# Optimization experiments

Hardware: AMD Instinct MI355X
Metric: run time of the kernel (lower is better)

## Reference

```python
import jax, jax.numpy as jnp
import numpy as np


def setup_inputs() -> dict:
    key = jax.random.key(0)
    ks = jax.random.split(key, 18)
    V, E, H, T = 32000, 512, 1024, 256
    s_e = 1.0 / np.sqrt(E)
    s_h = 1.0 / np.sqrt(H)
    inp = {
        "encoding": jax.random.normal(ks[0], (1, H), jnp.float32),
        "tokens": jax.random.randint(ks[1], (T,), 0, V),
        "embedding": jax.random.normal(ks[2], (V, E), jnp.float32),
        "wzx_w": jax.random.normal(ks[3], (H, E), jnp.float32) * s_e,
        "wzx_b": jax.random.normal(ks[4], (H,), jnp.float32) * s_e,
        "wrx_w": jax.random.normal(ks[5], (H, E), jnp.float32) * s_e,
        "wrx_b": jax.random.normal(ks[6], (H,), jnp.float32) * s_e,
        "whx_w": jax.random.normal(ks[7], (H, E), jnp.float32) * s_e,
        "whx_b": jax.random.normal(ks[8], (H,), jnp.float32) * s_e,
        "wzh_w": jax.random.normal(ks[9], (H, H), jnp.float32) * s_h,
        "wzh_b": jax.random.normal(ks[10], (H,), jnp.float32) * s_h,
        "wrh_w": jax.random.normal(ks[11], (H, H), jnp.float32) * s_h,
        "wrh_b": jax.random.normal(ks[12], (H,), jnp.float32) * s_h,
        "whh_w": jax.random.normal(ks[13], (H, H), jnp.float32) * s_h,
        "whh_b": jax.random.normal(ks[14], (H,), jnp.float32) * s_h,
        "out_w": jax.random.normal(ks[15], (V, H), jnp.float32) * s_h,
        "out_b": jax.random.normal(ks[16], (V,), jnp.float32) * s_h,
    }
    return inp


def reference(encoding, tokens, embedding,
              wzx_w, wzx_b, wrx_w, wrx_b, whx_w, whx_b,
              wzh_w, wzh_b, wrh_w, wrh_b, whh_w, whh_b,
              out_w, out_b):
    # Teacher-forced GRU decode: tokens[t] is the 'previous word' fed at step t.
    def step(h, tok):
        e = embedding[tok][None, :]                                   # [1, E]
        z = jax.nn.sigmoid(e @ wzx_w.T + wzx_b + h @ wzh_w.T + wzh_b)  # [1, H]
        r = jax.nn.sigmoid(e @ wrx_w.T + wrx_b + h @ wrh_w.T + wrh_b)
        h_prime = jnp.tanh(e @ whx_w.T + whx_b + (r * h) @ whh_w.T + whh_b)
        h_new = (1.0 - z) * h + z * h_prime
        logits = h_new @ out_w.T + out_b                               # [1, V]
        return h_new, logits

    _, output_vectors = jax.lax.scan(step, encoding, tokens)          # [T, 1, V]
    pred_ids = jnp.argmax(output_vectors, axis=-1)                    # [T, 1]
    return output_vectors, pred_ids
```

## Files before the change

kernel.cpp:

```cpp
#include <hip/hip_runtime.h>
#include <hip/hip_bf16.h>
#include <math.h>

constexpr int T_STEPS = 256;
constexpr int HDIM    = 1024;
constexpr int EDIM    = 512;
constexpr int VDIM    = 32000;

#define RG     128
#define RROWS  8

constexpr size_t WS_BZ     = 0;
constexpr size_t WS_BR     = WS_BZ + (size_t)T_STEPS * HDIM;
constexpr size_t WS_A      = WS_BR + (size_t)T_STEPS * HDIM;
constexpr size_t WS_HPACK  = WS_A  + (size_t)T_STEPS * HDIM;
constexpr size_t WS_RHPACK = WS_HPACK + (size_t)2 * (T_STEPS + 1) * HDIM;
constexpr size_t WS_HSEQ   = WS_BZ;
constexpr size_t WS_HSEQB  = WS_BR;

typedef __attribute__((ext_vector_type(8))) short short8;
typedef __attribute__((ext_vector_type(4))) float f32x4;

__device__ __forceinline__ float sigmoidf_(float x) { return 1.0f / (1.0f + __expf(-x)); }

__device__ __forceinline__ unsigned long long pack_tv(int tag, float v) {
  return ((unsigned long long)(unsigned)tag << 32) | (unsigned long long)__float_as_uint(v);
}

__device__ __forceinline__ unsigned short f2bf(float f) {
  unsigned u = __float_as_uint(f);
  return (unsigned short)((u + 0x7FFFu + ((u >> 16) & 1u)) >> 16);
}

__global__ __launch_bounds__(256) void k_init(const float* __restrict__ enc, float* __restrict__ ws) {
  unsigned long long* hpack  = (unsigned long long*)(ws + WS_HPACK);
  unsigned long long* rhpack = (unsigned long long*)(ws + WS_RHPACK);
  const int b = blockIdx.x, tid = threadIdx.x;
  if (b == 0) {
    for (int i = tid; i < HDIM; i += 256) hpack[i] = pack_tv(1, enc[i]);
  } else if (b <= T_STEPS) {
    unsigned long long* row = hpack + (size_t)b * HDIM;
    for (int i = tid; i < HDIM; i += 256) row[i] = 0ULL;
  } else {
    for (int i = tid; i < HDIM; i += 256) rhpack[i] = 0ULL;
  }
}

__global__ __launch_bounds__(256) void k_xproj(
    const int* __restrict__ tokens, const float* __restrict__ emb,
    const float* __restrict__ wzx, const float* __restrict__ wrx, const float* __restrict__ whx,
    const float* __restrict__ bzx, const float* __restrict__ bzh,
    const float* __restrict__ brx, const float* __restrict__ brh,
    const float* __restrict__ bhx, const float* __restrict__ bhh,
    float* __restrict__ ws) {
  __shared__ __align__(16) float es[16][EDIM];
  const int b   = blockIdx.x;
  const int t0  = (b & 15) * 16;
  const int c   = b >> 4;
  const int tid = threadIdx.x;

  {
    int row = tid >> 4;
    int kc  = (tid & 15) * 32;
    int tok = tokens[t0 + row];
    const float4* ep = (const float4*)(emb + (size_t)tok * EDIM + kc);
    float4* dst = (float4*)&es[row][kc];
    #pragma unroll
    for (int q = 0; q < 8; q++) dst[q] = ep[q];
  }
  __syncthreads();

  const int mat = c >> 2;
  const int j   = (c & 3) * 256 + tid;
  const float* W; const float* b1; const float* b2; float* Xout;
  if (mat == 0)      { W = wzx; b1 = bzx; b2 = bzh; Xout = ws + WS_BZ; }
  else if (mat == 1) { W = wrx; b1 = brx; b2 = brh; Xout = ws + WS_BR; }
  else               { W = whx; b1 = bhx; b2 = bhh; Xout = ws + WS_A;  }

  const float4* wp = (const float4*)(W + (size_t)j * EDIM);
  const float bias = b1[j] + b2[j];
  float acc[16];
  #pragma unroll
  for (int tt = 0; tt < 16; tt++) acc[tt] = 0.0f;

  for (int k4 = 0; k4 < EDIM / 4; k4++) {
    float4 w = wp[k4];
    #pragma unroll
    for (int tt = 0; tt < 16; tt++) {
      float4 e4 = *(const float4*)&es[tt][k4 * 4];
      acc[tt] += w.x * e4.x + w.y * e4.y + w.z * e4.z + w.w * e4.w;
    }
  }
  #pragma unroll
  for (int tt = 0; tt < 16; tt++)
    Xout[(size_t)(t0 + tt) * HDIM + j] = acc[tt] + bias;
}

__global__ __launch_bounds__(256) void k_recur(
    const float* __restrict__ wzh, const float* __restrict__ wrh, const float* __restrict__ whh,
    float* __restrict__ ws) {
  const int g    = blockIdx.x;
  const int tid  = threadIdx.x;
  const int lane = tid & 63;
  const int wv   = tid >> 6;
  const float* Bz = ws + WS_BZ;
  const float* Br = ws + WS_BR;
  const float* Aa = ws + WS_A;
  float* hseq = ws + WS_HSEQ;
  unsigned short* hseqb = (unsigned short*)(ws + WS_HSEQB);
  unsigned long long* hpack  = (unsigned long long*)(ws + WS_HPACK);
  unsigned long long* rhpack = (unsigned long long*)(ws + WS_RHPACK);

  const int j0 = 4 * tid;
  const int r0 = g * RROWS;

  float4 wz[RROWS], wr[RROWS], wh[RROWS];
  #pragma unroll
  for (int k = 0; k < RROWS; k++) {
    wz[k] = *(const float4*)(wzh + (size_t)(r0 + k) * HDIM + j0);
    wr[k] = *(const float4*)(wrh + (size_t)(r0 + k) * HDIM + j0);
    wh[k] = *(const float4*)(whh + (size_t)(r0 + k) * HDIM + j0);
  }

  __shared__ float redA[4][2 * RROWS];
  __shared__ float redB[4][RROWS];
  __shared__ float zs[RROWS];
  __shared__ float hloc[RROWS];
  if (tid < RROWS)
    hloc[tid] = __uint_as_float((unsigned)hpack[r0 + tid]);
  __syncthreads();

  for (int t = 0; t < T_STEPS; t++) {
    float bz_pre = 0.0f, br_pre = 0.0f, a_pre = 0.0f;
    if (tid < RROWS) {
      bz_pre = Bz[(size_t)t * HDIM + r0 + tid];
      a_pre  = Aa[(size_t)t * HDIM + r0 + tid];
    } else if (tid < 2 * RROWS) {
      br_pre = Br[(size_t)t * HDIM + r0 + (tid - RROWS)];
    }
    const unsigned long long ex = (unsigned long long)(unsigned)(t + 1);

    float hv0, hv1, hv2, hv3;
    {
      const unsigned long long* hp = hpack + (size_t)t * HDIM + j0;
      unsigned long long w0, w1, w2, w3;
      int it = 0;
      for (;;) {
        w0 = __hip_atomic_load(hp + 0, __ATOMIC_RELAXED, __HIP_MEMORY_SCOPE_AGENT);
        if ((w0 >> 32) == ex) break;
        if (++it > (1 << 20)) break;
        __builtin_amdgcn_s_sleep(2);
      }
      for (;;) {
        w1 = __hip_atomic_load(hp + 1, __ATOMIC_RELAXED, __HIP_MEMORY_SCOPE_AGENT);
        w2 = __hip_atomic_load(hp + 2, __ATOMIC_RELAXED, __HIP_MEMORY_SCOPE_AGENT);
        w3 = __hip_atomic_load(hp + 3, __ATOMIC_RELAXED, __HIP_MEMORY_SCOPE_AGENT);
        if (((w1 >> 32) == ex) & ((w2 >> 32) == ex) & ((w3 >> 32) == ex)) break;
        if (++it > (1 << 20)) break;
        __builtin_amdgcn_s_sleep(1);
      }
      hv0 = __uint_as_float((unsigned)w0);
      hv1 = __uint_as_float((unsigned)w1);
      hv2 = __uint_as_float((unsigned)w2);
      hv3 = __uint_as_float((unsigned)w3);
    }

    float pz[RROWS], pr[RROWS];
    #pragma unroll
    for (int k = 0; k < RROWS; k++) {
      pz[k] = wz[k].x * hv0 + wz[k].y * hv1 + wz[k].z * hv2 + wz[k].w * hv3;
      pr[k] = wr[k].x * hv0 + wr[k].y * hv1 + wr[k].z * hv2 + wr[k].w * hv3;
    }
    #pragma unroll
    for (int m = 32; m >= 1; m >>= 1) {
      #pragma unroll
      for (int k = 0; k < RROWS; k++) {
        pz[k] += __shfl_xor(pz[k], m);
        pr[k] += __shfl_xor(pr[k], m);
      }
    }
    if (lane == 0) {
      #pragma unroll
      for (int k = 0; k < RROWS; k++) { redA[wv][k] = pz[k]; redA[wv][RROWS + k] = pr[k]; }
    }
    __syncthreads();
    if (tid < RROWS) {
      float u = redA[0][tid] + redA[1][tid] + redA[2][tid] + redA[3][tid];
      zs[tid] = sigmoidf_(bz_pre + u);
    } else if (tid < 2 * RROWS) {
      int k = tid - RROWS;
      float u = redA[0][tid] + redA[1][tid] + redA[2][tid] + redA[3][tid];
      float r = sigmoidf_(br_pre + u);
      float rh = r * hloc[k];
      __hip_atomic_store(&rhpack[r0 + k], pack_tv(t + 1, rh),
                         __ATOMIC_RELAXED, __HIP_MEMORY_SCOPE_AGENT);
    }

    float rv0, rv1, rv2, rv3;
    {
      const unsigned long long* rp = rhpack + j0;
      unsigned long long w0, w1, w2, w3;
      int it = 0;
      for (;;) {
        w0 = __hip_atomic_load(rp + 0, __ATOMIC_RELAXED, __HIP_MEMORY_SCOPE_AGENT);
        if ((w0 >> 32) == ex) break;
        if (++it > (1 << 20)) break;
        __builtin_amdgcn_s_sleep(2);
      }
      for (;;) {
        w1 = __hip_atomic_load(rp + 1, __ATOMIC_RELAXED, __HIP_MEMORY_SCOPE_AGENT);
        w2 = __hip_atomic_load(rp + 2, __ATOMIC_RELAXED, __HIP_MEMORY_SCOPE_AGENT);
        w3 = __hip_atomic_load(rp + 3, __ATOMIC_RELAXED, __HIP_MEMORY_SCOPE_AGENT);
        if (((w1 >> 32) == ex) & ((w2 >> 32) == ex) & ((w3 >> 32) == ex)) break;
        if (++it > (1 << 20)) break;
        __builtin_amdgcn_s_sleep(1);
      }
      rv0 = __uint_as_float((unsigned)w0);
      rv1 = __uint_as_float((unsigned)w1);
      rv2 = __uint_as_float((unsigned)w2);
      rv3 = __uint_as_float((unsigned)w3);
    }

    float ph[RROWS];
    #pragma unroll
    for (int k = 0; k < RROWS; k++)
      ph[k] = wh[k].x * rv0 + wh[k].y * rv1 + wh[k].z * rv2 + wh[k].w * rv3;
    #pragma unroll
    for (int m = 32; m >= 1; m >>= 1) {
      #pragma unroll
      for (int k = 0; k < RROWS; k++) ph[k] += __shfl_xor(ph[k], m);
    }
    if (lane == 0) {
      #pragma unroll
      for (int k = 0; k < RROWS; k++) redB[wv][k] = ph[k];
    }
    __syncthreads();
    if (tid < RROWS) {
      float v  = redB[0][tid] + redB[1][tid] + redB[2][tid] + redB[3][tid];
      float z  = zs[tid];
      float hk = hloc[tid];
      float hp_ = tanhf(a_pre + v);
      float hn = (1.0f - z) * hk + z * hp_;
      hloc[tid] = hn;
      __hip_atomic_store(&hpack[(size_t)(t + 1) * HDIM + r0 + tid], pack_tv(t + 2, hn),
                         __ATOMIC_RELAXED, __HIP_MEMORY_SCOPE_AGENT);
      hseq[(size_t)t * HDIM + r0 + tid] = hn;
      hseqb[(size_t)t * HDIM + r0 + tid] = f2bf(hn);
    }
  }
}

__global__ __launch_bounds__(256) void k_gemm(
    const unsigned short* __restrict__ Abf, const float* __restrict__ outw,
    const float* __restrict__ outb, float* __restrict__ out) {
  const int tid  = threadIdx.x;
  const int lane = tid & 63;
  const int wv   = tid >> 6;
  const int n0   = blockIdx.x * 128;
  const int rA   = lane & 15;
  const int kg   = lane >> 4;

  f32x4 acc[4][8];
  #pragma unroll
  for (int i = 0; i < 4; i++)
    #pragma unroll
    for (int j = 0; j < 8; j++) acc[i][j] = (f32x4){0.f, 0.f, 0.f, 0.f};

  const int mbase = wv * 64 + rA;

  for (int k0 = 0; k0 < HDIM; k0 += 32) {
    const int ks = k0 + kg * 8;
    short8 afr[4];
    #pragma unroll
    for (int i = 0; i < 4; i++)
      afr[i] = *(const short8*)(Abf + (size_t)(mbase + i * 16) * HDIM + ks);

    short8 bfr[8];
    #pragma unroll
    for (int j = 0; j < 8; j++) {
      const float* bp = outw + (size_t)(n0 + j * 16 + rA) * HDIM + ks;
      float4 b0 = *(const float4*)(bp);
      float4 b1 = *(const float4*)(bp + 4);
      short8 s;
      s[0] = (short)f2bf(b0.x); s[1] = (short)f2bf(b0.y);
      s[2] = (short)f2bf(b0.z); s[3] = (short)f2bf(b0.w);
      s[4] = (short)f2bf(b1.x); s[5] = (short)f2bf(b1.y);
      s[6] = (short)f2bf(b1.z); s[7] = (short)f2bf(b1.w);
      bfr[j] = s;
    }

    #pragma unroll
    for (int i = 0; i < 4; i++)
      #pragma unroll
      for (int j = 0; j < 8; j++)
        acc[i][j] = __builtin_amdgcn_mfma_f32_16x16x32_bf16(afr[i], bfr[j], acc[i][j], 0, 0, 0);
  }

  float bias[8];
  #pragma unroll
  for (int j = 0; j < 8; j++) bias[j] = outb[n0 + j * 16 + rA];
  #pragma unroll
  for (int i = 0; i < 4; i++) {
    #pragma unroll
    for (int j = 0; j < 8; j++) {
      #pragma unroll
      for (int r = 0; r < 4; r++) {
        int m = wv * 64 + i * 16 + kg * 4 + r;
        out[(size_t)m * VDIM + n0 + j * 16 + rA] = acc[i][j][r] + bias[j];
      }
    }
  }
}

__global__ __launch_bounds__(256) void k_argmax(const float* __restrict__ logits,
                                                const float* __restrict__ hseqf,
                                                const float* __restrict__ outw,
                                                const float* __restrict__ outb,
                                                float* __restrict__ outids) {
  const int t = blockIdx.x;
  const int tid = threadIdx.x;
  const float* row = logits + (size_t)t * VDIM;

  float mx = -3.4e38f;
  for (int v = tid; v < VDIM; v += 256) mx = fmaxf(mx, row[v]);
  __shared__ float sm[256];
  sm[tid] = mx;
  __syncthreads();
  for (int s = 128; s > 0; s >>= 1) {
    if (tid < s) sm[tid] = fmaxf(sm[tid], sm[tid + s]);
    __syncthreads();
  }
  const float bmax = sm[0];
  __syncthreads();

  __shared__ int cand[64];
  __shared__ int cnt;
  if (tid == 0) cnt = 0;
  __syncthreads();
  const float cut = bmax - 0.25f;
  for (int v = tid; v < VDIM; v += 256) {
    if (row[v] >= cut) {
      int p = atomicAdd(&cnt, 1);
      if (p < 64) cand[p] = v;
    }
  }
  __syncthreads();
  int n = cnt < 64 ? cnt : 64;

  __shared__ float cval[64];
  if (tid < n) {
    int v = cand[tid];
    const float* w = outw + (size_t)v * HDIM;
    const float* h = hseqf + (size_t)t * HDIM;
    float s0 = 0.f, s1 = 0.f, s2 = 0.f, s3 = 0.f;
    for (int k = 0; k < HDIM; k += 4) {
      float4 wf = *(const float4*)(w + k);
      float4 hf = *(const float4*)(h + k);
      s0 += wf.x * hf.x; s1 += wf.y * hf.y; s2 += wf.z * hf.z; s3 += wf.w * hf.w;
    }
    cval[tid] = (s0 + s1) + (s2 + s3) + outb[v];
  }
  __syncthreads();
  if (tid == 0) {
    float best = -3.4e38f; int bi = 0x7FFFFFFF;
    for (int i = 0; i < n; i++) {
      float v = cval[i]; int id = cand[i];
      if (v > best || (v == best && id < bi)) { best = v; bi = id; }
    }
    outids[t] = (float)bi;
  }
}

extern "C" void kernel_launch(void* const* d_in, const int* in_sizes, int n_in,
                              void* d_out, int out_size, void* d_ws, size_t ws_size,
                              hipStream_t stream) {
  (void)in_sizes; (void)n_in; (void)out_size; (void)ws_size;
  const float* enc    = (const float*)d_in[0];
  const int*   tokens = (const int*)d_in[1];
  const float* emb    = (const float*)d_in[2];
  const float* wzx_w  = (const float*)d_in[3];
  const float* wzx_b  = (const float*)d_in[4];
  const float* wrx_w  = (const float*)d_in[5];
  const float* wrx_b  = (const float*)d_in[6];
  const float* whx_w  = (const float*)d_in[7];
  const float* whx_b  = (const float*)d_in[8];
  const float* wzh_w  = (const float*)d_in[9];
  const float* wzh_b  = (const float*)d_in[10];
  const float* wrh_w  = (const float*)d_in[11];
  const float* wrh_b  = (const float*)d_in[12];
  const float* whh_w  = (const float*)d_in[13];
  const float* whh_b  = (const float*)d_in[14];
  const float* out_w  = (const float*)d_in[15];
  const float* out_b  = (const float*)d_in[16];
  float* ws  = (float*)d_ws;
  float* out = (float*)d_out;

  k_init<<<dim3(T_STEPS + 2), dim3(256), 0, stream>>>(enc, ws);
  k_xproj<<<dim3(192), dim3(256), 0, stream>>>(tokens, emb, wzx_w, wrx_w, whx_w,
                                               wzx_b, wzh_b, wrx_b, wrh_b, whx_b, whh_b, ws);
  k_recur<<<dim3(RG), dim3(256), 0, stream>>>(wzh_w, wrh_w, whh_w, ws);
  k_gemm<<<dim3(VDIM / 128), dim3(256), 0, stream>>>((const unsigned short*)(ws + WS_HSEQB),
                                                     out_w, out_b, out);
  k_argmax<<<dim3(T_STEPS), dim3(256), 0, stream>>>(out, ws + WS_HSEQ, out_w, out_b,
                                                    out + (size_t)T_STEPS * VDIM);
}
```

Baseline: 1.435 ms.

## Assign two rows per wave in recurrence kernel, dropping block barriers

The recurrent kernel now gives each wavefront two whole output rows. Each wave reduces its dot products with warp shuffles only, which removes the shared-memory reductions and both __syncthreads per step. Weights are no longer kept in registers; each wave reloads its rows of wzh/wrh/whh from global memory (likely L2-resident) every step, overlapping the loads with the spin-wait. Every lane now polls 16 packed h values instead of 4, which adds polling traffic, and the spin timeout is shortened.

Result: slower. 2.909 ms (+102.7%).

```diff
diff --git a/kernel.cpp b/kernel.cpp
--- a/kernel.cpp
+++ b/kernel.cpp
@@ -103,6 +103,9 @@
   const int tid  = threadIdx.x;
   const int lane = tid & 63;
   const int wv   = tid >> 6;
+  const int row0 = g * RROWS + 2 * wv;
+  const int row1 = row0 + 1;
+
   const float* Bz = ws + WS_BZ;
   const float* Br = ws + WS_BR;
   const float* Aa = ws + WS_A;
@@ -111,141 +114,138 @@
   unsigned long long* hpack  = (unsigned long long*)(ws + WS_HPACK);
   unsigned long long* rhpack = (unsigned long long*)(ws + WS_RHPACK);
 
-  const int j0 = 4 * tid;
-  const int r0 = g * RROWS;
-
-  float4 wz[RROWS], wr[RROWS], wh[RROWS];
-  #pragma unroll
-  for (int k = 0; k < RROWS; k++) {
-    wz[k] = *(const float4*)(wzh + (size_t)(r0 + k) * HDIM + j0);
-    wr[k] = *(const float4*)(wrh + (size_t)(r0 + k) * HDIM + j0);
-    wh[k] = *(const float4*)(whh + (size_t)(r0 + k) * HDIM + j0);
-  }
-
-  __shared__ float redA[4][2 * RROWS];
-  __shared__ float redB[4][RROWS];
-  __shared__ float zs[RROWS];
-  __shared__ float hloc[RROWS];
-  if (tid < RROWS)
-    hloc[tid] = __uint_as_float((unsigned)hpack[r0 + tid]);
-  __syncthreads();
+  const int c0 = 4 * lane;
+
+  float hl0 = __uint_as_float((unsigned)hpack[row0]);
+  float hl1 = __uint_as_float((unsigned)hpack[row1]);
 
   for (int t = 0; t < T_STEPS; t++) {
-    float bz_pre = 0.0f, br_pre = 0.0f, a_pre = 0.0f;
-    if (tid < RROWS) {
-      bz_pre = Bz[(size_t)t * HDIM + r0 + tid];
-      a_pre  = Aa[(size_t)t * HDIM + r0 + tid];
-    } else if (tid < 2 * RROWS) {
-      br_pre = Br[(size_t)t * HDIM + r0 + (tid - RROWS)];
-    }
     const unsigned long long ex = (unsigned long long)(unsigned)(t + 1);
 
-    float hv0, hv1, hv2, hv3;
+    float br0 = Br[(size_t)t * HDIM + row0], br1 = Br[(size_t)t * HDIM + row1];
+    float bz0 = Bz[(size_t)t * HDIM + row0], bz1 = Bz[(size_t)t * HDIM + row1];
+    float a0  = Aa[(size_t)t * HDIM + row0], a1  = Aa[(size_t)t * HDIM + row1];
+
+    float4 WZ0[4], WZ1[4], WR0[4], WR1[4];
+    #pragma unroll
+    for (int q = 0; q < 4; q++) {
+      const int col = c0 + 256 * q;
+      WZ0[q] = *(const float4*)(wzh + (size_t)row0 * HDIM + col);
+      WZ1[q] = *(const float4*)(wzh + (size_t)row1 * HDIM + col);
+      WR0[q] = *(const float4*)(wrh + (size_t)row0 * HDIM + col);
+      WR1[q] = *(const float4*)(wrh + (size_t)row1 * HDIM + col);
+    }
+
+    unsigned long long hw[16];
     {
-      const unsigned long long* hp = hpack + (size_t)t * HDIM + j0;
-      unsigned long long w0, w1, w2, w3;
+      const unsigned long long* hp = hpack + (size_t)t * HDIM;
       int it = 0;
       for (;;) {
-        w0 = __hip_atomic_load(hp + 0, __ATOMIC_RELAXED, __HIP_MEMORY_SCOPE_AGENT);
-        if ((w0 >> 32) == ex) break;
-        if (++it > (1 << 20)) break;
-        __builtin_amdgcn_s_sleep(2);
-      }
-      for (;;) {
-        w1 = __hip_atomic_load(hp + 1, __ATOMIC_RELAXED, __HIP_MEMORY_SCOPE_AGENT);
-        w2 = __hip_atomic_load(hp + 2, __ATOMIC_RELAXED, __HIP_MEMORY_SCOPE_AGENT);
-        w3 = __hip_atomic_load(hp + 3, __ATOMIC_RELAXED, __HIP_MEMORY_SCOPE_AGENT);
-        if (((w1 >> 32) == ex) & ((w2 >> 32) == ex) & ((w3 >> 32) == ex)) break;
-        if (++it > (1 << 20)) break;
+        #pragma unroll
+        for (int q = 0; q < 4; q++)
+          #pragma unroll
+          for (int c = 0; c < 4; c++)
+            hw[q * 4 + c] = __hip_atomic_load(hp + c0 + 256 * q + c,
+                                              __ATOMIC_RELAXED, __HIP_MEMORY_SCOPE_AGENT);
+        bool ok = true;
+        #pragma unroll
+        for (int i = 0; i < 16; i++) ok &= ((hw[i] >> 32) == ex);
+        if (ok) break;
+        if (++it > (1 << 14)) break;
         __builtin_amdgcn_s_sleep(1);
       }
-      hv0 = __uint_as_float((unsigned)w0);
-      hv1 = __uint_as_float((unsigned)w1);
-      hv2 = __uint_as_float((unsigned)w2);
-      hv3 = __uint_as_float((unsigned)w3);
-    }
-
-    float pz[RROWS], pr[RROWS];
-    #pragma unroll
-    for (int k = 0; k < RROWS; k++) {
-      pz[k] = wz[k].x * hv0 + wz[k].y * hv1 + wz[k].z * hv2 + wz[k].w * hv3;
-      pr[k] = wr[k].x * hv0 + wr[k].y * hv1 + wr[k].z * hv2 + wr[k].w * hv3;
-    }
+    }
+
+    float accz0 = 0.f, accz1 = 0.f, accr0 = 0.f, accr1 = 0.f;
+    #pragma unroll
+    for (int q = 0; q < 4; q++) {
+      const float h0 = __uint_as_float((unsigned)hw[q * 4 + 0]);
+      const float h1 = __uint_as_float((unsigned)hw[q * 4 + 1]);
+      const float h2 = __uint_as_float((unsigned)hw[q * 4 + 2]);
+      const float h3 = __uint_as_float((unsigned)hw[q * 4 + 3]);
+      accr0 += WR0[q].x * h0 + WR0[q].y * h1 + WR0[q].z * h2 + WR0[q].w * h3;
+      accr1 += WR1[q].x * h0 + WR1[q].y * h1 + WR1[q].z * h2 + WR1[q].w * h3;
+      accz0 += WZ0[q].x * h0 + WZ0[q].y * h1 + WZ0[q].z * h2 + WZ0[q].w * h3;
+      accz1 += WZ1[q].x * h0 + WZ1[q].y * h1 + WZ1[q].z * h2 + WZ1[q].w * h3;
+    }
+
+    float4 WH0[4], WH1[4];
+    #pragma unroll
+    for (int q = 0; q < 4; q++) {
+      const int col = c0 + 256 * q;
+      WH0[q] = *(const float4*)(whh + (size_t)row0 * HDIM + col);
+      WH1[q] = *(const float4*)(whh + (size_t)row1 * HDIM + col);
+    }
+
     #pragma unroll
     for (int m = 32; m >= 1; m >>= 1) {
-      #pragma unroll
-      for (int k = 0; k < RROWS; k++) {
-        pz[k] += __shfl_xor(pz[k], m);
-        pr[k] += __shfl_xor(pr[k], m);
-      }
-    }
+      accr0 += __shfl_xor(accr0, m);
+      accr1 += __shfl_xor(accr1, m);
+    }
+    const float r0 = sigmoidf_(br0 + accr0);
+    const float r1 = sigmoidf_(br1 + accr1);
     if (lane == 0) {
-      #pragma unroll
-      for (int k = 0; k < RROWS; k++) { redA[wv][k] = pz[k]; redA[wv][RROWS + k] = pr[k]; }
-    }
-    __syncthreads();
-    if (tid < RROWS) {
-      float u = redA[0][tid] + redA[1][tid] + redA[2][tid] + redA[3][tid];
-      zs[tid] = sigmoidf_(bz_pre + u);
-    } else if (tid < 2 * RROWS) {
-      int k = tid - RROWS;
-      float u = redA[0][tid] + redA[1][tid] + redA[2][tid] + redA[3][tid];
-      float r = sigmoidf_(br_pre + u);
-      float rh = r * hloc[k];
-      __hip_atomic_store(&rhpack[r0 + k], pack_tv(t + 1, rh),
+      __hip_atomic_store(&rhpack[row0], pack_tv(t + 1, r0 * hl0),
                          __ATOMIC_RELAXED, __HIP_MEMORY_SCOPE_AGENT);
-    }
-
-    float rv0, rv1, rv2, rv3;
+      __hip_atomic_store(&rhpack[row1], pack_tv(t + 1, r1 * hl1),
+                         __ATOMIC_RELAXED, __HIP_MEMORY_SCOPE_AGENT);
+    }
+    #pragma unroll
+    for (int m = 32; m >= 1; m >>= 1) {
+      accz0 += __shfl_xor(accz0, m);
+      accz1 += __shfl_xor(accz1, m);
+    }
+    const float z0 = sigmoidf_(bz0 + accz0);
+    const float z1 = sigmoidf_(bz1 + accz1);
+
+    unsigned long long rw[16];
     {
-      const unsigned long long* rp = rhpack + j0;
-      unsigned long long w0, w1, w2, w3;
       int it = 0;
       for (;;) {
-        w0 = __hip_atomic_load(rp + 0, __ATOMIC_RELAXED, __HIP_MEMORY_SCOPE_AGENT);
-        if ((w0 >> 32) == ex) break;
-        if (++it > (1 << 20)) break;
-        __builtin_amdgcn_s_sleep(2);
-      }
-      for (;;) {
-        w1 = __hip_atomic_load(rp + 1, __ATOMIC_RELAXED, __HIP_MEMORY_SCOPE_AGENT);
-        w2 = __hip_atomic_load(rp + 2, __ATOMIC_RELAXED, __HIP_MEMORY_SCOPE_AGENT);
-        w3 = __hip_atomic_load(rp + 3, __ATOMIC_RELAXED, __HIP_MEMORY_SCOPE_AGENT);
-        if (((w1 >> 32) == ex) & ((w2 >> 32) == ex) & ((w3 >> 32) == ex)) break;
-        if (++it > (1 << 20)) break;
+        #pragma unroll
+        for (int q = 0; q < 4; q++)
+          #pragma unroll
+          for (int c = 0; c < 4; c++)
+            rw[q * 4 + c] = __hip_atomic_load(rhpack + c0 + 256 * q + c,
+                                              __ATOMIC_RELAXED, __HIP_MEMORY_SCOPE_AGENT);
+        bool ok = true;
+        #pragma unroll
+        for (int i = 0; i < 16; i++) ok &= ((rw[i] >> 32) == ex);
+        if (ok) break;
+        if (++it > (1 << 14)) break;
         __builtin_amdgcn_s_sleep(1);
       }
-      rv0 = __uint_as_float((unsigned)w0);
-      rv1 = __uint_as_float((unsigned)w1);
-      rv2 = __uint_as_float((unsigned)w2);
-      rv3 = __uint_as_float((unsigned)w3);
-    }
-
-    float ph[RROWS];
-    #pragma unroll
-    for (int k = 0; k < RROWS; k++)
-      ph[k] = wh[k].x * rv0 + wh[k].y * rv1 + wh[k].z * rv2 + wh[k].w * rv3;
+    }
+
+    float accv0 = 0.f, accv1 = 0.f;
+    #pragma unroll
+    for (int q = 0; q < 4; q++) {
+      const float v0 = __uint_as_float((unsigned)rw[q * 4 + 0]);
+      const float v1 = __uint_as_float((unsigned)rw[q * 4 + 1]);
+      const float v2 = __uint_as_float((unsigned)rw[q * 4 + 2]);
+      const float v3 = __uint_as_float((unsigned)rw[q * 4 + 3]);
+      accv0 += WH0[q].x * v0 + WH0[q].y * v1 + WH0[q].z * v2 + WH0[q].w * v3;
+      accv1 += WH1[q].x * v0 + WH1[q].y * v1 + WH1[q].z * v2 + WH1[q].w * v3;
+    }
     #pragma unroll
     for (int m = 32; m >= 1; m >>= 1) {
-      #pragma unroll
-      for (int k = 0; k < RROWS; k++) ph[k] += __shfl_xor(ph[k], m);
-    }
+      accv0 += __shfl_xor(accv0, m);
+      accv1 += __shfl_xor(accv1, m);
+    }
+    const float hp0 = tanhf(a0 + accv0);
+    const float hp1 = tanhf(a1 + accv1);
+    const float hn0 = (1.0f - z0) * hl0 + z0 * hp0;
+    const float hn1 = (1.0f - z1) * hl1 + z1 * hp1;
+    hl0 = hn0; hl1 = hn1;
+
     if (lane == 0) {
-      #pragma unroll
-      for (int k = 0; k < RROWS; k++) redB[wv][k] = ph[k];
-    }
-    __syncthreads();
-    if (tid < RROWS) {
-      float v  = redB[0][tid] + redB[1][tid] + redB[2][tid] + redB[3][tid];
-      float z  = zs[tid];
-      float hk = hloc[tid];
-      float hp_ = tanhf(a_pre + v);
-      float hn = (1.0f - z) * hk + z * hp_;
-      hloc[tid] = hn;
-      __hip_atomic_store(&hpack[(size_t)(t + 1) * HDIM + r0 + tid], pack_tv(t + 2, hn),
+      __hip_atomic_store(&hpack[(size_t)(t + 1) * HDIM + row0], pack_tv(t + 2, hn0),
                          __ATOMIC_RELAXED, __HIP_MEMORY_SCOPE_AGENT);
-      hseq[(size_t)t * HDIM + r0 + tid] = hn;
-      hseqb[(size_t)t * HDIM + r0 + tid] = f2bf(hn);
+      __hip_atomic_store(&hpack[(size_t)(t + 1) * HDIM + row1], pack_tv(t + 2, hn1),
+                         __ATOMIC_RELAXED, __HIP_MEMORY_SCOPE_AGENT);
+      *(float2*)(hseq + (size_t)t * HDIM + row0) = make_float2(hn0, hn1);
+      unsigned pk = (unsigned)f2bf(hn0) | ((unsigned)f2bf(hn1) << 16);
+      *(unsigned*)(hseqb + (size_t)t * HDIM + row0) = pk;
     }
   }
 }
```
